# Kernel optimization log

Measured on AMD Instinct MI355X. Metric: run time of the kernel, lower is better.

## Reference

```python
import jax, jax.numpy as jnp
import numpy as np


def setup_inputs() -> dict:
    key = jax.random.key(0)
    k1, k2 = jax.random.split(key)
    B, C, R, I, O = 64, 16, 1152, 64, 64
    x = jax.random.normal(k1, (B, R, I), dtype=jnp.float32)
    route_weights = jax.random.normal(k2, (C, R, I, O), dtype=jnp.float32)
    route_logits = jnp.zeros((C, 1, R, 1, 1), dtype=jnp.float32)
    return {"x": x, "route_weights": route_weights, "route_logits": route_logits}


def _squash(t, axis=-1):
    # scale = |t|^2 / (1 + |t|^2); out = scale * t / |t|  (no epsilon, faithful to source)
    sq = jnp.sum(t * t, axis=axis, keepdims=True)
    return (sq / (1.0 + sq)) * t / jnp.sqrt(sq)


def reference(x, route_weights, route_logits):
    NUM_ITERS = 3
    # priors: (C, B, R, 1, O)
    priors = jnp.einsum('bri,crio->cbro', x, route_weights)[:, :, :, None, :]
    logits = route_logits  # (C, 1, R, 1, 1), broadcasts over batch
    outputs = None
    for i in range(NUM_ITERS):
        probs = jax.nn.softmax(logits, axis=2)          # softmax over route nodes
        s = jnp.sum(probs * priors, axis=2, keepdims=True)  # (C, B, 1, 1, O)
        outputs = _squash(s, axis=-1)
        if i != NUM_ITERS - 1:
            # delta logits: agreement between priors and outputs
            logits = logits + jnp.sum(priors * outputs, axis=-1, keepdims=True)
    return outputs  # (C, B, 1, 1, O)
```

## Files before the change

### kernel.cpp

```cpp
#include <hip/hip_runtime.h>
#include <math.h>

#define Cc 16
#define Bb 64
#define Rr 1152
#define Ii 64
#define Oo 64
#define CH 4
#define NRB 128
#define RT 9
#define RTF 8

static __device__ __forceinline__ float4 ld4(const float* p){ return *reinterpret_cast<const float4*>(p); }
static __device__ __forceinline__ void st4(float* p, float4 v){ *reinterpret_cast<float4*>(p) = v; }

static __device__ __forceinline__ void gl_lds16(const float4* g, float4* l){
  __builtin_amdgcn_global_load_lds(
      (const __attribute__((address_space(1))) void*)g,
      (__attribute__((address_space(3))) void*)l, 16, 0, 0);
}

__device__ float gProbs0[Cc*Rr];
__device__ float gS[Cc*Bb*Oo];
__device__ float gOut[Cc*Bb*Oo];
__device__ float gL1[(size_t)Cc*Bb*Rr];
__device__ float gLp[(size_t)Cc*Bb*Rr];

__global__ void kz_zeroS(){
  const int i = blockIdx.x*256 + threadIdx.x;
  if (i < Cc*Bb*Oo) gS[i] = 0.f;
}

static __device__ void softmax_row(const float* __restrict__ L, float* __restrict__ out,
                                   float* __restrict__ sred){
  const int tid = threadIdx.x;
  float m = -3.4e38f;
  for (int r = tid; r < Rr; r += 256) m = fmaxf(m, L[r]);
  #pragma unroll
  for (int off = 1; off < 64; off <<= 1) m = fmaxf(m, __shfl_xor(m, off));
  if ((tid & 63) == 0) sred[tid >> 6] = m;
  __syncthreads();
  m = fmaxf(fmaxf(sred[0], sred[1]), fmaxf(sred[2], sred[3]));
  float s = 0.f;
  for (int r = tid; r < Rr; r += 256) s += __expf(L[r] - m);
  #pragma unroll
  for (int off = 1; off < 64; off <<= 1) s += __shfl_xor(s, off);
  if ((tid & 63) == 0) sred[4 + (tid >> 6)] = s;
  __syncthreads();
  s = sred[4] + sred[5] + sred[6] + sred[7];
  const float inv = 1.0f / s;
  for (int r = tid; r < Rr; r += 256) out[r] = __expf(L[r] - m) * inv;
}

__global__ void k0f(const float* __restrict__ lg){
  __shared__ float sred[8];
  softmax_row(lg + blockIdx.x*Rr, gProbs0 + blockIdx.x*Rr, sred);
}
__global__ void k0p(const float* __restrict__ lg, float* __restrict__ pr){
  __shared__ float sred[8];
  softmax_row(lg + blockIdx.x*Rr, pr + blockIdx.x*Rr, sred);
}

static __device__ __forceinline__ void fma_row(float4& a, const float4 xv,
    const float4 w0, const float4 w1, const float4 w2, const float4 w3){
  a.x = fmaf(xv.x, w0.x, fmaf(xv.y, w1.x, fmaf(xv.z, w2.x, fmaf(xv.w, w3.x, a.x))));
  a.y = fmaf(xv.x, w0.y, fmaf(xv.y, w1.y, fmaf(xv.z, w2.y, fmaf(xv.w, w3.y, a.y))));
  a.z = fmaf(xv.x, w0.z, fmaf(xv.y, w1.z, fmaf(xv.z, w2.z, fmaf(xv.w, w3.z, a.z))));
  a.w = fmaf(xv.x, w0.w, fmaf(xv.y, w1.w, fmaf(xv.z, w2.w, fmaf(xv.w, w3.w, a.w))));
}

static __device__ __forceinline__ void stage_async(const float4* __restrict__ xsrc,
    const float4* __restrict__ wsrc, int r, int wv, int ln,
    float4* __restrict__ Wb, float4* __restrict__ Xb){
  #pragma unroll
  for (int qq = 0; qq < 4; ++qq) {
    const int base = (wv*4 + qq) * 64;
    const int p    = base + ln;
    gl_lds16(wsrc + p, Wb + base);
    const int b  = p >> 4;
    const int lc = (p & 15) ^ ((b >> 2) & 3);
    gl_lds16(xsrc + (((size_t)(b*Rr + r)) << 4) + lc, Xb + base);
  }
}

__launch_bounds__(256)
__global__ void k1_priors(const float* __restrict__ x, const float* __restrict__ w,
                          const float* __restrict__ probs0, int c0,
                          float* __restrict__ P, float* __restrict__ Sp){
  const int ci  = blockIdx.x;
  const int c   = c0 + ci;
  const int rb  = blockIdx.y;
  const int r0  = rb * RT;
  const int tid = threadIdx.x;
  const int q   = tid & 15;
  const int to  = q * 4;
  const int tb  = (tid >> 4) * 4;
  const int wv  = tid >> 6;
  const int ln  = tid & 63;
  const int sx  = (tb >> 2) & 3;

  __shared__ float4 Wl[2][1024];
  __shared__ float4 Xl[2][1024];

  const float4* xsrc = reinterpret_cast<const float4*>(x);

  float4 s0a[4];
  #pragma unroll
  for (int j = 0; j < 4; ++j) s0a[j] = make_float4(0.f,0.f,0.f,0.f);

  int buf = 0;
  stage_async(xsrc, reinterpret_cast<const float4*>(w) + (size_t)(c*Rr + r0)*1024,
              r0, wv, ln, Wl[0], Xl[0]);
  __syncthreads();

  for (int rr = 0; rr < RT; ++rr) {
    const int r = r0 + rr;
    if (rr + 1 < RT)
      stage_async(xsrc, reinterpret_cast<const float4*>(w) + (size_t)(c*Rr + r + 1)*1024,
                  r + 1, wv, ln, Wl[buf^1], Xl[buf^1]);

    const float4* W4 = Wl[buf];
    const float4* X4 = Xl[buf];
    float4 acc0 = make_float4(0.f,0.f,0.f,0.f);
    float4 acc1 = acc0, acc2 = acc0, acc3 = acc0;

    #pragma unroll
    for (int kg = 0; kg < 16; ++kg) {
      const float4 wv0 = W4[(kg*4+0)*16 + q];
      const float4 wv1 = W4[(kg*4+1)*16 + q];
      const float4 wv2 = W4[(kg*4+2)*16 + q];
      const float4 wv3 = W4[(kg*4+3)*16 + q];
      const int xc = kg ^ sx;
      const float4 xv0 = X4[(tb+0)*16 + xc];
      const float4 xv1 = X4[(tb+1)*16 + xc];
      const float4 xv2 = X4[(tb+2)*16 + xc];
      const float4 xv3 = X4[(tb+3)*16 + xc];
      fma_row(acc0, xv0, wv0, wv1, wv2, wv3);
      fma_row(acc1, xv1, wv0, wv1, wv2, wv3);
      fma_row(acc2, xv2, wv0, wv1, wv2, wv3);
      fma_row(acc3, xv3, wv0, wv1, wv2, wv3);
    }

    const float pr = probs0[c*Rr + r];
    st4(&P[(((size_t)(ci*Bb + tb+0))*Rr + r)*Oo + to], acc0);
    st4(&P[(((size_t)(ci*Bb + tb+1))*Rr + r)*Oo + to], acc1);
    st4(&P[(((size_t)(ci*Bb + tb+2))*Rr + r)*Oo + to], acc2);
    st4(&P[(((size_t)(ci*Bb + tb+3))*Rr + r)*Oo + to], acc3);
    s0a[0].x = fmaf(pr, acc0.x, s0a[0].x); s0a[0].y = fmaf(pr, acc0.y, s0a[0].y);
    s0a[0].z = fmaf(pr, acc0.z, s0a[0].z); s0a[0].w = fmaf(pr, acc0.w, s0a[0].w);
    s0a[1].x = fmaf(pr, acc1.x, s0a[1].x); s0a[1].y = fmaf(pr, acc1.y, s0a[1].y);
    s0a[1].z = fmaf(pr, acc1.z, s0a[1].z); s0a[1].w = fmaf(pr, acc1.w, s0a[1].w);
    s0a[2].x = fmaf(pr, acc2.x, s0a[2].x); s0a[2].y = fmaf(pr, acc2.y, s0a[2].y);
    s0a[2].z = fmaf(pr, acc2.z, s0a[2].z); s0a[2].w = fmaf(pr, acc2.w, s0a[2].w);
    s0a[3].x = fmaf(pr, acc3.x, s0a[3].x); s0a[3].y = fmaf(pr, acc3.y, s0a[3].y);
    s0a[3].z = fmaf(pr, acc3.z, s0a[3].z); s0a[3].w = fmaf(pr, acc3.w, s0a[3].w);

    __syncthreads();
    buf ^= 1;
  }

  #pragma unroll
  for (int j = 0; j < 4; ++j)
    st4(&Sp[((((size_t)ci*NRB) + rb)*Bb + tb + j)*Oo + to], s0a[j]);
}

__launch_bounds__(256)
__global__ void k2_reduce(const float* __restrict__ Sp, float* __restrict__ out0){
  const int blk = blockIdx.x;
  const int ci  = blk >> 6, b = blk & 63;
  const int wv  = threadIdx.x >> 6, o = threadIdx.x & 63;
  __shared__ float part[4][64];
  float s = 0.f;
  #pragma unroll 4
  for (int rb = wv*32; rb < wv*32 + 32; ++rb)
    s += Sp[((((size_t)ci*NRB) + rb)*Bb + b)*Oo + o];
  part[wv][o] = s;
  __syncthreads();
  if (threadIdx.x < 64) {
    s = part[0][o] + part[1][o] + part[2][o] + part[3][o];
    float t2 = s*s;
    #pragma unroll
    for (int off = 1; off < 64; off <<= 1) t2 += __shfl_xor(t2, off);
    out0[(size_t)blk*Oo + o] = s * (t2 / ((1.0f + t2) * sqrtf(t2)));
  }
}

__launch_bounds__(512)
__global__ void k3_routing(const float* __restrict__ P, const float* __restrict__ out0,
                           const float* __restrict__ lg0g, int c0,
                           float* __restrict__ out){
  const int b   = blockIdx.x;
  const int ci  = blockIdx.y;
  const int c   = c0 + ci;
  const int tid = threadIdx.x;
  const int wv  = tid >> 6;
  const int ln  = tid & 63;
  const int g   = ln >> 4;
  const int q   = ln & 15;
  const int o4  = q * 4;
  const int pid = wv*4 + g;

  __shared__ float lg0[Rr];
  __shared__ float lgs1[Rr];
  __shared__ float outv[Oo];
  __shared__ float marr[32], larr[32];
  __shared__ float sarr[32*Oo];

  for (int r = tid; r < Rr; r += 512) lg0[r] = lg0g[c*Rr + r];
  if (tid < 64) outv[tid] = out0[((size_t)(ci*Bb + b))*Oo + tid];
  __syncthreads();

  const float4* Pcb = reinterpret_cast<const float4*>(P) + ((size_t)(ci*Bb + b))*Rr*16;
  const int rbase = wv*4 + g;

  #pragma unroll 1
  for (int pass = 1; pass <= 2; ++pass) {
    float m = -3.4e38f, l = 0.f;
    float4 sa = make_float4(0.f,0.f,0.f,0.f);
    const float4 ov = ld4(&outv[o4]);

    #pragma unroll 1
    for (int it = 0; it < 9; ++it) {
      const int r0i = it*128 + rbase;
      const float4 pv0 = Pcb[(r0i +  0)*16 + q];
      const float4 pv1 = Pcb[(r0i + 32)*16 + q];
      const float4 pv2 = Pcb[(r0i + 64)*16 + q];
      const float4 pv3 = Pcb[(r0i + 96)*16 + q];

      float d0 = pv0.x*ov.x + pv0.y*ov.y + pv0.z*ov.z + pv0.w*ov.w;
      float d1 = pv1.x*ov.x + pv1.y*ov.y + pv1.z*ov.z + pv1.w*ov.w;
      float d2 = pv2.x*ov.x + pv2.y*ov.y + pv2.z*ov.z + pv2.w*ov.w;
      float d3 = pv3.x*ov.x + pv3.y*ov.y + pv3.z*ov.z + pv3.w*ov.w;
      #pragma unroll
      for (int off = 1; off < 16; off <<= 1) {
        d0 += __shfl_xor(d0, off);
        d1 += __shfl_xor(d1, off);
        d2 += __shfl_xor(d2, off);
        d3 += __shfl_xor(d3, off);
      }
      float b0, b1, b2, b3;
      if (pass == 1) { b0 = lg0[r0i]; b1 = lg0[r0i+32]; b2 = lg0[r0i+64]; b3 = lg0[r0i+96]; }
      else           { b0 = lgs1[r0i]; b1 = lgs1[r0i+32]; b2 = lgs1[r0i+64]; b3 = lgs1[r0i+96]; }
      const float l0 = b0 + d0, l1 = b1 + d1, l2 = b2 + d2, l3 = b3 + d3;
      if (pass == 1 && q == 0) {
        lgs1[r0i] = l0; lgs1[r0i+32] = l1; lgs1[r0i+64] = l2; lgs1[r0i+96] = l3;
      }
      const float mx = fmaxf(fmaxf(fmaxf(l0, l1), fmaxf(l2, l3)), m);
      const float wo = __expf(m - mx);
      const float e0 = __expf(l0 - mx), e1 = __expf(l1 - mx);
      const float e2 = __expf(l2 - mx), e3 = __expf(l3 - mx);
      l = l*wo + e0 + e1 + e2 + e3;
      sa.x = fmaf(pv0.x, e0, fmaf(pv1.x, e1, fmaf(pv2.x, e2, fmaf(pv3.x, e3, sa.x*wo))));
      sa.y = fmaf(pv0.y, e0, fmaf(pv1.y, e1, fmaf(pv2.y, e2, fmaf(pv3.y, e3, sa.y*wo))));
      sa.z = fmaf(pv0.z, e0, fmaf(pv1.z, e1, fmaf(pv2.z, e2, fmaf(pv3.z, e3, sa.z*wo))));
      sa.w = fmaf(pv0.w, e0, fmaf(pv1.w, e1, fmaf(pv2.w, e2, fmaf(pv3.w, e3, sa.w*wo))));
      m = mx;
    }

    if (q == 0) { marr[pid] = m; larr[pid] = l; }
    st4(&sarr[pid*Oo + o4], sa);
    __syncthreads();

    if (tid < 64) {
      float M = -3.4e38f;
      #pragma unroll
      for (int p = 0; p < 32; ++p) M = fmaxf(M, marr[p]);
      float L = 0.f, sv = 0.f;
      #pragma unroll
      for (int p = 0; p < 32; ++p) {
        const float f = __expf(marr[p] - M);
        L += larr[p] * f;
        sv = fmaf(sarr[p*Oo + tid], f, sv);
      }
      const float s = sv / L;
      float t2 = s*s;
      #pragma unroll
      for (int off = 1; off < 64; off <<= 1) t2 += __shfl_xor(t2, off);
      outv[tid] = s * (t2 / ((1.0f + t2) * sqrtf(t2)));
    }
    __syncthreads();
  }

  if (tid < 64) out[((size_t)c*Bb + b)*Oo + tid] = outv[tid];
}

static __device__ void stage_gemm(const float* __restrict__ x, const float* __restrict__ w,
                                  int c, int r, int tid, int tb, int to,
                                  float* __restrict__ Xs, float* __restrict__ Ws,
                                  float4* __restrict__ acc){
  const float4* wsrc = reinterpret_cast<const float4*>(w + (size_t)(c*Rr + r) * (Ii*Oo));
  #pragma unroll
  for (int qq = 0; qq < 4; ++qq) {
    const int fi = tid + 256*qq;
    reinterpret_cast<float4*>(Ws)[fi] = wsrc[fi];
    const int b  = fi >> 4;
    const int i4 = (fi & 15) << 2;
    st4(&Xs[b*68 + i4], ld4(x + (size_t)(b*Rr + r)*Ii + i4));
  }
  __syncthreads();
  #pragma unroll
  for (int j = 0; j < 4; ++j) acc[j] = make_float4(0.f,0.f,0.f,0.f);
  #pragma unroll
  for (int i4 = 0; i4 < Ii; i4 += 4) {
    const float4 xv0 = ld4(&Xs[(tb+0)*68 + i4]);
    const float4 xv1 = ld4(&Xs[(tb+1)*68 + i4]);
    const float4 xv2 = ld4(&Xs[(tb+2)*68 + i4]);
    const float4 xv3 = ld4(&Xs[(tb+3)*68 + i4]);
    const float4 wv0 = ld4(&Ws[(i4+0)*64 + to]);
    const float4 wv1 = ld4(&Ws[(i4+1)*64 + to]);
    const float4 wv2 = ld4(&Ws[(i4+2)*64 + to]);
    const float4 wv3 = ld4(&Ws[(i4+3)*64 + to]);
    fma_row(acc[0], xv0, wv0, wv1, wv2, wv3);
    fma_row(acc[1], xv1, wv0, wv1, wv2, wv3);
    fma_row(acc[2], xv2, wv0, wv1, wv2, wv3);
    fma_row(acc[3], xv3, wv0, wv1, wv2, wv3);
  }
}

__launch_bounds__(256)
__global__ void kf_sum(const float* __restrict__ x, const float* __restrict__ w, int which){
  const int c = blockIdx.x, r0 = blockIdx.y * RTF, tid = threadIdx.x;
  const int to = (tid & 15) * 4, tb = (tid >> 4) * 4;
  __shared__ float Xs[64*68];
  __shared__ float Ws[64*64];
  const float* pcbr = (which == 1) ? gLp : gL1;
  float4 sa[4];
  #pragma unroll
  for (int j = 0; j < 4; ++j) sa[j] = make_float4(0.f,0.f,0.f,0.f);
  for (int rr = 0; rr < RTF; ++rr) {
    const int r = r0 + rr;
    float4 acc[4];
    stage_gemm(x, w, c, r, tid, tb, to, Xs, Ws, acc);
    #pragma unroll
    for (int j = 0; j < 4; ++j) {
      const float wt = (which == 0) ? gProbs0[c*Rr + r]
                                    : pcbr[(size_t)(c*Bb + tb + j)*Rr + r];
      sa[j].x = fmaf(wt, acc[j].x, sa[j].x);
      sa[j].y = fmaf(wt, acc[j].y, sa[j].y);
      sa[j].z = fmaf(wt, acc[j].z, sa[j].z);
      sa[j].w = fmaf(wt, acc[j].w, sa[j].w);
    }
    __syncthreads();
  }
  #pragma unroll
  for (int j = 0; j < 4; ++j) {
    float* dst = &gS[(size_t)(c*Bb + tb + j)*Oo + to];
    atomicAdd(dst + 0, sa[j].x);
    atomicAdd(dst + 1, sa[j].y);
    atomicAdd(dst + 2, sa[j].z);
    atomicAdd(dst + 3, sa[j].w);
  }
}

__launch_bounds__(256)
__global__ void kf_delta(const float* __restrict__ x, const float* __restrict__ w,
                         const float* __restrict__ lg, int pass){
  const int c = blockIdx.x, r0 = blockIdx.y * RTF, tid = threadIdx.x;
  const int to = (tid & 15) * 4, tb = (tid >> 4) * 4;
  __shared__ float Xs[64*68];
  __shared__ float Ws[64*64];
  float* dst = (pass == 1) ? gL1 : gLp;
  float4 ov[4];
  #pragma unroll
  for (int j = 0; j < 4; ++j) ov[j] = ld4(&gOut[(size_t)(c*Bb + tb + j)*Oo + to]);
  for (int rr = 0; rr < RTF; ++rr) {
    const int r = r0 + rr;
    float4 acc[4];
    stage_gemm(x, w, c, r, tid, tb, to, Xs, Ws, acc);
    float pd[4];
    #pragma unroll
    for (int j = 0; j < 4; ++j) {
      float d = acc[j].x*ov[j].x + acc[j].y*ov[j].y + acc[j].z*ov[j].z + acc[j].w*ov[j].w;
      d += __shfl_xor(d, 1); d += __shfl_xor(d, 2);
      d += __shfl_xor(d, 4); d += __shfl_xor(d, 8);
      pd[j] = d;
    }
    if ((tid & 15) == 0) {
      #pragma unroll
      for (int j = 0; j < 4; ++j) {
        const size_t li = (size_t)(c*Bb + tb + j)*Rr + r;
        const float base = (pass == 1) ? lg[c*Rr + r] : gL1[li];
        dst[li] = base + pd[j];
      }
    }
    __syncthreads();
  }
}

__global__ void kf_softmax(int dir){
  __shared__ float sred[8];
  const size_t idx = blockIdx.x;
  const float* src = (dir == 0) ? gL1 : gLp;
  float*       dst = (dir == 0) ? gLp : gL1;
  softmax_row(src + idx*Rr, dst + idx*Rr, sred);
}

__global__ void kf_squash(float* __restrict__ out, int toFinal){
  const size_t idx = blockIdx.x;
  const int t = threadIdx.x;
  const float s = gS[idx*Oo + t];
  float t2 = s*s;
  #pragma unroll
  for (int off = 1; off < 64; off <<= 1) t2 += __shfl_xor(t2, off);
  float* dst = toFinal ? out : gOut;
  dst[idx*Oo + t] = s * (t2 / ((1.0f + t2) * sqrtf(t2)));
}

extern "C" void kernel_launch(void* const* d_in, const int* in_sizes, int n_in,
                              void* d_out, int out_size, void* d_ws, size_t ws_size,
                              hipStream_t stream) {
  const float* x  = (const float*)d_in[0];
  const float* w  = (const float*)d_in[1];
  const float* lg = (const float*)d_in[2];
  float* out = (float*)d_out;
  float* ws  = (float*)d_ws;

  const size_t nP  = (size_t)CH*Bb*Rr*Oo;
  const size_t nSp = (size_t)CH*NRB*Bb*Oo;
  const size_t nO0 = (size_t)CH*Bb*Oo;
  const size_t nPr = (size_t)Cc*Rr;
  const size_t need = (nP + nSp + nO0 + nPr) * sizeof(float);

  if (ws_size >= need) {
    float* P   = ws;
    float* Sp  = P + nP;
    float* o0  = Sp + nSp;
    float* pr  = o0 + nO0;
    k0p<<<dim3(Cc), 256, 0, stream>>>(lg, pr);
    for (int c0 = 0; c0 < Cc; c0 += CH) {
      k1_priors<<<dim3(CH, NRB), 256, 0, stream>>>(x, w, pr, c0, P, Sp);
      k2_reduce<<<dim3(CH*Bb), 256, 0, stream>>>(Sp, o0);
      k3_routing<<<dim3(Bb, CH), 512, 0, stream>>>(P, o0, lg, c0, out);
    }
  } else {
    const dim3 gTiles(Cc, Rr/RTF);
    const int  zb = (Cc*Bb*Oo + 255)/256;
    kz_zeroS<<<dim3(zb), 256, 0, stream>>>();
    k0f<<<dim3(Cc), 256, 0, stream>>>(lg);
    kf_sum   <<<gTiles, 256, 0, stream>>>(x, w, 0);
    kf_squash<<<dim3(Cc*Bb), 64, 0, stream>>>(out, 0);
    kf_delta <<<gTiles, 256, 0, stream>>>(x, w, lg, 1);
    kf_softmax<<<dim3(Cc*Bb), 256, 0, stream>>>(0);
    kz_zeroS <<<dim3(zb), 256, 0, stream>>>();
    kf_sum   <<<gTiles, 256, 0, stream>>>(x, w, 1);
    kf_squash<<<dim3(Cc*Bb), 64, 0, stream>>>(out, 0);
    kf_delta <<<gTiles, 256, 0, stream>>>(x, w, lg, 2);
    kf_softmax<<<dim3(Cc*Bb), 256, 0, stream>>>(1);
    kz_zeroS <<<dim3(zb), 256, 0, stream>>>();
    kf_sum   <<<gTiles, 256, 0, stream>>>(x, w, 2);
    kf_squash<<<dim3(Cc*Bb), 64, 0, stream>>>(out, 1);
  }
}
```

Before: 632.3 us.

## Use register-staged prefetch in priors GEMM, larger chunks, wider routing blocks

The priors kernel stops using async global-to-LDS loads into a double buffer. It now prefetches the next route's weights (with nontemporal loads) and x into registers, then writes them into a single LDS buffer between two barriers. Chunk size grows from 4 to 8 capsules and route tiles shrink from 9 to 4, which gives more blocks per launch and fewer launches. The routing kernel moves to 1024 threads with 64 partial groups, each handling 3 rows per step. The costs are an extra barrier per step, more registers held for the prefetch, a larger priors workspace, and a longer partial-sum reduction.

```diff
diff --git a/kernel.cpp b/kernel.cpp
--- a/kernel.cpp
+++ b/kernel.cpp
@@ -6,18 +6,18 @@
 #define Rr 1152
 #define Ii 64
 #define Oo 64
-#define CH 4
-#define NRB 128
-#define RT 9
+#define CH 8
+#define RT 4
+#define NRB 288
 #define RTF 8
+
+typedef float f4v __attribute__((ext_vector_type(4)));
 
 static __device__ __forceinline__ float4 ld4(const float* p){ return *reinterpret_cast<const float4*>(p); }
 static __device__ __forceinline__ void st4(float* p, float4 v){ *reinterpret_cast<float4*>(p) = v; }
-
-static __device__ __forceinline__ void gl_lds16(const float4* g, float4* l){
-  __builtin_amdgcn_global_load_lds(
-      (const __attribute__((address_space(1))) void*)g,
-      (__attribute__((address_space(3))) void*)l, 16, 0, 0);
+static __device__ __forceinline__ float4 ntld4(const float4* p){
+  f4v v = __builtin_nontemporal_load(reinterpret_cast<const f4v*>(p));
+  float4 r; r.x = v.x; r.y = v.y; r.z = v.z; r.w = v.w; return r;
 }
 
 __device__ float gProbs0[Cc*Rr];
@@ -69,17 +69,27 @@
   a.w = fmaf(xv.x, w0.w, fmaf(xv.y, w1.w, fmaf(xv.z, w2.w, fmaf(xv.w, w3.w, a.w))));
 }
 
-static __device__ __forceinline__ void stage_async(const float4* __restrict__ xsrc,
-    const float4* __restrict__ wsrc, int r, int wv, int ln,
-    float4* __restrict__ Wb, float4* __restrict__ Xb){
+struct Stage { float4 wv[4]; float4 xv[4]; };
+
+static __device__ __forceinline__ void issue_loads(const float4* __restrict__ wsrcR,
+    const float4* __restrict__ xsrc, int r, int tid, Stage& st){
   #pragma unroll
   for (int qq = 0; qq < 4; ++qq) {
-    const int base = (wv*4 + qq) * 64;
-    const int p    = base + ln;
-    gl_lds16(wsrc + p, Wb + base);
-    const int b  = p >> 4;
-    const int lc = (p & 15) ^ ((b >> 2) & 3);
-    gl_lds16(xsrc + (((size_t)(b*Rr + r)) << 4) + lc, Xb + base);
+    const int p = tid + 256*qq;
+    st.wv[qq] = ntld4(wsrcR + p);
+    const int b = p >> 4, col = p & 15;
+    st.xv[qq] = ld4((const float*)(xsrc + ((size_t)(b*Rr + r) << 4) + col));
+  }
+}
+
+static __device__ __forceinline__ void write_lds(float4* __restrict__ Wl, float4* __restrict__ Xl,
+                                                 int tid, const Stage& st){
+  #pragma unroll
+  for (int qq = 0; qq < 4; ++qq) {
+    const int p = tid + 256*qq;
+    Wl[p] = st.wv[qq];
+    const int b = p >> 4, col = p & 15;
+    Xl[b*16 + (col ^ (b >> 2))] = st.xv[qq];
   }
 }
 
@@ -94,47 +104,42 @@
   const int tid = threadIdx.x;
   const int q   = tid & 15;
   const int to  = q * 4;
-  const int tb  = (tid >> 4) * 4;
-  const int wv  = tid >> 6;
-  const int ln  = tid & 63;
-  const int sx  = (tb >> 2) & 3;
-
-  __shared__ float4 Wl[2][1024];
-  __shared__ float4 Xl[2][1024];
+  const int g   = tid >> 4;
+  const int tb  = g * 4;
+
+  __shared__ float4 Wl[1024];
+  __shared__ float4 Xl[1024];
 
   const float4* xsrc = reinterpret_cast<const float4*>(x);
+  const float4* wbase = reinterpret_cast<const float4*>(w) + (size_t)c*Rr*1024;
 
   float4 s0a[4];
   #pragma unroll
   for (int j = 0; j < 4; ++j) s0a[j] = make_float4(0.f,0.f,0.f,0.f);
 
-  int buf = 0;
-  stage_async(xsrc, reinterpret_cast<const float4*>(w) + (size_t)(c*Rr + r0)*1024,
-              r0, wv, ln, Wl[0], Xl[0]);
+  Stage st;
+  issue_loads(wbase + (size_t)r0*1024, xsrc, r0, tid, st);
+  write_lds(Wl, Xl, tid, st);
   __syncthreads();
 
   for (int rr = 0; rr < RT; ++rr) {
     const int r = r0 + rr;
-    if (rr + 1 < RT)
-      stage_async(xsrc, reinterpret_cast<const float4*>(w) + (size_t)(c*Rr + r + 1)*1024,
-                  r + 1, wv, ln, Wl[buf^1], Xl[buf^1]);
-
-    const float4* W4 = Wl[buf];
-    const float4* X4 = Xl[buf];
+    const bool more = (rr + 1 < RT);
+    if (more) issue_loads(wbase + (size_t)(r+1)*1024, xsrc, r+1, tid, st);
+
     float4 acc0 = make_float4(0.f,0.f,0.f,0.f);
     float4 acc1 = acc0, acc2 = acc0, acc3 = acc0;
-
     #pragma unroll
     for (int kg = 0; kg < 16; ++kg) {
-      const float4 wv0 = W4[(kg*4+0)*16 + q];
-      const float4 wv1 = W4[(kg*4+1)*16 + q];
-      const float4 wv2 = W4[(kg*4+2)*16 + q];
-      const float4 wv3 = W4[(kg*4+3)*16 + q];
-      const int xc = kg ^ sx;
-      const float4 xv0 = X4[(tb+0)*16 + xc];
-      const float4 xv1 = X4[(tb+1)*16 + xc];
-      const float4 xv2 = X4[(tb+2)*16 + xc];
-      const float4 xv3 = X4[(tb+3)*16 + xc];
+      const float4 wv0 = Wl[(kg*4+0)*16 + q];
+      const float4 wv1 = Wl[(kg*4+1)*16 + q];
+      const float4 wv2 = Wl[(kg*4+2)*16 + q];
+      const float4 wv3 = Wl[(kg*4+3)*16 + q];
+      const int xc = kg ^ g;
+      const float4 xv0 = Xl[(tb+0)*16 + xc];
+      const float4 xv1 = Xl[(tb+1)*16 + xc];
+      const float4 xv2 = Xl[(tb+2)*16 + xc];
+      const float4 xv3 = Xl[(tb+3)*16 + xc];
       fma_row(acc0, xv0, wv0, wv1, wv2, wv3);
       fma_row(acc1, xv1, wv0, wv1, wv2, wv3);
       fma_row(acc2, xv2, wv0, wv1, wv2, wv3);
@@ -155,8 +160,11 @@
     s0a[3].x = fmaf(pr, acc3.x, s0a[3].x); s0a[3].y = fmaf(pr, acc3.y, s0a[3].y);
     s0a[3].z = fmaf(pr, acc3.z, s0a[3].z); s0a[3].w = fmaf(pr, acc3.w, s0a[3].w);
 
-    __syncthreads();
-    buf ^= 1;
+    if (more) {
+      __syncthreads();
+      write_lds(Wl, Xl, tid, st);
+      __syncthreads();
+    }
   }
 
   #pragma unroll
@@ -171,8 +179,7 @@
   const int wv  = threadIdx.x >> 6, o = threadIdx.x & 63;
   __shared__ float part[4][64];
   float s = 0.f;
-  #pragma unroll 4
-  for (int rb = wv*32; rb < wv*32 + 32; ++rb)
+  for (int rb = wv*(NRB/4); rb < (wv+1)*(NRB/4); ++rb)
     s += Sp[((((size_t)ci*NRB) + rb)*Bb + b)*Oo + o];
   part[wv][o] = s;
   __syncthreads();
@@ -185,7 +192,7 @@
   }
 }
 
-__launch_bounds__(512)
+__launch_bounds__(1024)
 __global__ void k3_routing(const float* __restrict__ P, const float* __restrict__ out0,
                            const float* __restrict__ lg0g, int c0,
                            float* __restrict__ out){
@@ -195,23 +202,22 @@
   const int tid = threadIdx.x;
   const int wv  = tid >> 6;
   const int ln  = tid & 63;
-  const int g   = ln >> 4;
+  const int gw  = ln >> 4;
   const int q   = ln & 15;
   const int o4  = q * 4;
-  const int pid = wv*4 + g;
+  const int G   = wv*4 + gw;
 
   __shared__ float lg0[Rr];
   __shared__ float lgs1[Rr];
   __shared__ float outv[Oo];
-  __shared__ float marr[32], larr[32];
-  __shared__ float sarr[32*Oo];
-
-  for (int r = tid; r < Rr; r += 512) lg0[r] = lg0g[c*Rr + r];
+  __shared__ float marr[64], larr[64];
+  __shared__ float sarr[64*Oo];
+
+  for (int r = tid; r < Rr; r += 1024) lg0[r] = lg0g[c*Rr + r];
   if (tid < 64) outv[tid] = out0[((size_t)(ci*Bb + b))*Oo + tid];
   __syncthreads();
 
   const float4* Pcb = reinterpret_cast<const float4*>(P) + ((size_t)(ci*Bb + b))*Rr*16;
-  const int rbase = wv*4 + g;
 
   #pragma unroll 1
   for (int pass = 1; pass <= 2; ++pass) {
@@ -220,54 +226,48 @@
     const float4 ov = ld4(&outv[o4]);
 
     #pragma unroll 1
-    for (int it = 0; it < 9; ++it) {
-      const int r0i = it*128 + rbase;
-      const float4 pv0 = Pcb[(r0i +  0)*16 + q];
-      const float4 pv1 = Pcb[(r0i + 32)*16 + q];
-      const float4 pv2 = Pcb[(r0i + 64)*16 + q];
-      const float4 pv3 = Pcb[(r0i + 96)*16 + q];
+    for (int j6 = 0; j6 < 6; ++j6) {
+      const int r0i = G + 192*j6;
+      const float4 pv0 = Pcb[(r0i +   0)*16 + q];
+      const float4 pv1 = Pcb[(r0i +  64)*16 + q];
+      const float4 pv2 = Pcb[(r0i + 128)*16 + q];
 
       float d0 = pv0.x*ov.x + pv0.y*ov.y + pv0.z*ov.z + pv0.w*ov.w;
       float d1 = pv1.x*ov.x + pv1.y*ov.y + pv1.z*ov.z + pv1.w*ov.w;
       float d2 = pv2.x*ov.x + pv2.y*ov.y + pv2.z*ov.z + pv2.w*ov.w;
-      float d3 = pv3.x*ov.x + pv3.y*ov.y + pv3.z*ov.z + pv3.w*ov.w;
       #pragma unroll
       for (int off = 1; off < 16; off <<= 1) {
         d0 += __shfl_xor(d0, off);
         d1 += __shfl_xor(d1, off);
         d2 += __shfl_xor(d2, off);
-        d3 += __shfl_xor(d3, off);
       }
-      float b0, b1, b2, b3;
-      if (pass == 1) { b0 = lg0[r0i]; b1 = lg0[r0i+32]; b2 = lg0[r0i+64]; b3 = lg0[r0i+96]; }
-      else           { b0 = lgs1[r0i]; b1 = lgs1[r0i+32]; b2 = lgs1[r0i+64]; b3 = lgs1[r0i+96]; }
-      const float l0 = b0 + d0, l1 = b1 + d1, l2 = b2 + d2, l3 = b3 + d3;
-      if (pass == 1 && q == 0) {
-        lgs1[r0i] = l0; lgs1[r0i+32] = l1; lgs1[r0i+64] = l2; lgs1[r0i+96] = l3;
-      }
-      const float mx = fmaxf(fmaxf(fmaxf(l0, l1), fmaxf(l2, l3)), m);
+      float b0, b1, b2;
+      if (pass == 1) { b0 = lg0[r0i]; b1 = lg0[r0i+64]; b2 = lg0[r0i+128]; }
+      else           { b0 = lgs1[r0i]; b1 = lgs1[r0i+64]; b2 = lgs1[r0i+128]; }
+      const float l0 = b0 + d0, l1 = b1 + d1, l2 = b2 + d2;
+      if (pass == 1 && q == 0) { lgs1[r0i] = l0; lgs1[r0i+64] = l1; lgs1[r0i+128] = l2; }
+      const float mx = fmaxf(m, fmaxf(fmaxf(l0, l1), l2));
       const float wo = __expf(m - mx);
-      const float e0 = __expf(l0 - mx), e1 = __expf(l1 - mx);
-      const float e2 = __expf(l2 - mx), e3 = __expf(l3 - mx);
-      l = l*wo + e0 + e1 + e2 + e3;
-      sa.x = fmaf(pv0.x, e0, fmaf(pv1.x, e1, fmaf(pv2.x, e2, fmaf(pv3.x, e3, sa.x*wo))));
-      sa.y = fmaf(pv0.y, e0, fmaf(pv1.y, e1, fmaf(pv2.y, e2, fmaf(pv3.y, e3, sa.y*wo))));
-      sa.z = fmaf(pv0.z, e0, fmaf(pv1.z, e1, fmaf(pv2.z, e2, fmaf(pv3.z, e3, sa.z*wo))));
-      sa.w = fmaf(pv0.w, e0, fmaf(pv1.w, e1, fmaf(pv2.w, e2, fmaf(pv3.w, e3, sa.w*wo))));
+      const float e0 = __expf(l0 - mx), e1 = __expf(l1 - mx), e2 = __expf(l2 - mx);
+      l = l*wo + e0 + e1 + e2;
+      sa.x = fmaf(pv0.x, e0, fmaf(pv1.x, e1, fmaf(pv2.x, e2, sa.x*wo)));
+      sa.y = fmaf(pv0.y, e0, fmaf(pv1.y, e1, fmaf(pv2.y, e2, sa.y*wo)));
+      sa.z = fmaf(pv0.z, e0, fmaf(pv1.z, e1, fmaf(pv2.z, e2, sa.z*wo)));
+      sa.w = fmaf(pv0.w, e0, fmaf(pv1.w, e1, fmaf(pv2.w, e2, sa.w*wo)));
       m = mx;
     }
 
-    if (q == 0) { marr[pid] = m; larr[pid] = l; }
-    st4(&sarr[pid*Oo + o4], sa);
+    if (q == 0) { marr[G] = m; larr[G] = l; }
+    st4(&sarr[G*Oo + o4], sa);
     __syncthreads();
 
     if (tid < 64) {
       float M = -3.4e38f;
       #pragma unroll
-      for (int p = 0; p < 32; ++p) M = fmaxf(M, marr[p]);
+      for (int p = 0; p < 64; ++p) M = fmaxf(M, marr[p]);
       float L = 0.f, sv = 0.f;
-      #pragma unroll
-      for (int p = 0; p < 32; ++p) {
+      #pragma unroll 8
+      for (int p = 0; p < 64; ++p) {
         const float f = __expf(marr[p] - M);
         L += larr[p] * f;
         sv = fmaf(sarr[p*Oo + tid], f, sv);
@@ -430,7 +430,7 @@
     for (int c0 = 0; c0 < Cc; c0 += CH) {
       k1_priors<<<dim3(CH, NRB), 256, 0, stream>>>(x, w, pr, c0, P, Sp);
       k2_reduce<<<dim3(CH*Bb), 256, 0, stream>>>(Sp, o0);
-      k3_routing<<<dim3(Bb, CH), 512, 0, stream>>>(P, o0, lg, c0, out);
+      k3_routing<<<dim3(Bb, CH), 1024, 0, stream>>>(P, o0, lg, c0, out);
     }
   } else {
     const dim3 gTiles(Cc, Rr/RTF);
```

Result: faster. 585.4 us (-7.4%).
